# Performance work log

Measured on AMD Instinct MI355X. Metric: run time of the kernel, lower is better.

The kernel has to match this reference:

```python
import jax, jax.numpy as jnp
import numpy as np
from jax.ops import segment_sum

N, E, D, H = 50000, 800000, 128, 128


def setup_inputs() -> dict:
    key = jax.random.key(0)
    ks = jax.random.split(key, 8)
    x = jax.random.normal(ks[0], (N, D), dtype=jnp.float32)
    edge_index = jax.random.randint(ks[1], (2, E), 0, N, dtype=jnp.int64)
    # Glorot-ish scaled weights for 3 GCNConv layers
    s0 = 1.0 / np.sqrt(D)
    s1 = 1.0 / np.sqrt(H)
    W0 = jax.random.normal(ks[2], (D, H), dtype=jnp.float32) * s0
    W1 = jax.random.normal(ks[3], (H, H), dtype=jnp.float32) * s1
    W2 = jax.random.normal(ks[4], (H, H), dtype=jnp.float32) * s1
    b0 = jnp.zeros((H,), dtype=jnp.float32)
    b1 = jnp.zeros((H,), dtype=jnp.float32)
    b2 = jnp.zeros((H,), dtype=jnp.float32)
    return {"x": x, "edge_index": edge_index,
            "W0": W0, "b0": b0, "W1": W1, "b1": b1, "W2": W2, "b2": b2}


def _gcn_norm(edge_index, num_nodes):
    # Add self-loops, compute symmetric normalization deg^-1/2 A deg^-1/2
    loops = jnp.arange(num_nodes, dtype=edge_index.dtype)
    src = jnp.concatenate([edge_index[0], loops])  # [E+N]
    dst = jnp.concatenate([edge_index[1], loops])  # [E+N]
    deg = segment_sum(jnp.ones_like(dst, dtype=jnp.float32), dst,
                      num_segments=num_nodes)       # in-degree incl. self-loop
    dinv = jnp.where(deg > 0, jax.lax.rsqrt(deg), 0.0)
    norm = dinv[src] * dinv[dst]                    # [E+N]
    return src, dst, norm


def _gcn_conv(x, src, dst, norm, W, b, num_nodes):
    h = x @ W                                        # [N, H] linear first (PyG order)
    msg = h[src] * norm[:, None]                     # gather + scale
    agg = segment_sum(msg, dst, num_segments=num_nodes)  # scatter-add
    return agg + b


def reference(x, edge_index, W0, b0, W1, b1, W2, b2):
    num_nodes = x.shape[0]
    src, dst, norm = _gcn_norm(edge_index, num_nodes)
    for W, b in ((W0, b0), (W1, b1), (W2, b2)):
        x = jax.nn.relu(_gcn_conv(x, src, dst, norm, W, b, num_nodes))
    return x
```

## Files before the change

### kernel.cpp

```cpp
#include <hip/hip_runtime.h>


typedef __attribute__((ext_vector_type(8))) unsigned short ushort8;
typedef __attribute__((ext_vector_type(8))) short short8v;
typedef __attribute__((ext_vector_type(4))) float f32x4;

__device__ __forceinline__ unsigned short f2bf(float f) {
    unsigned u = __float_as_uint(f);
    unsigned r = (u + 0x7FFF + ((u >> 16) & 1)) >> 16;
    return (unsigned short)r;
}
__device__ __forceinline__ float bf2f(unsigned short s) {
    return __uint_as_float(((unsigned)s) << 16);
}

__global__ __launch_bounds__(256) void zero_kernel(int4* __restrict__ p, int n4) {
    int i = blockIdx.x * 256 + threadIdx.x;
    if (i < n4) p[i] = make_int4(0, 0, 0, 0);
}

__global__ void count_rank_kernel(const int* __restrict__ ei, int* __restrict__ cnt,
                                  int* __restrict__ rank, int E) {
    int e = (blockIdx.x * blockDim.x + threadIdx.x) * 4;
    if (e + 4 <= E) {
        int4 d4 = *(const int4*)(ei + E + e);
        int4 r;
        r.x = atomicAdd(&cnt[d4.x], 1);
        r.y = atomicAdd(&cnt[d4.y], 1);
        r.z = atomicAdd(&cnt[d4.z], 1);
        r.w = atomicAdd(&cnt[d4.w], 1);
        *(int4*)(rank + e) = r;
    } else {
        for (; e < E; ++e) rank[e] = atomicAdd(&cnt[ei[E + e]], 1);
    }
}

__global__ __launch_bounds__(256) void block_sum_kernel(const int* __restrict__ cnt,
                                                        int* __restrict__ bsum, int n) {
    int i = blockIdx.x * 256 + threadIdx.x;
    int v = (i < n) ? cnt[i] : 0;
#pragma unroll
    for (int off = 32; off; off >>= 1) v += __shfl_down(v, off);
    __shared__ int ws[4];
    int lane = threadIdx.x & 63, w = threadIdx.x >> 6;
    if (lane == 0) ws[w] = v;
    __syncthreads();
    if (threadIdx.x == 0) bsum[blockIdx.x] = ws[0] + ws[1] + ws[2] + ws[3];
}

__global__ __launch_bounds__(256) void scan_partials_kernel(const int* __restrict__ bsum,
                                                            int* __restrict__ bpre,
                                                            int* __restrict__ rowptr,
                                                            int nb, int n) {
    __shared__ int sh[256];
    int t = threadIdx.x;
    int v = (t < nb) ? bsum[t] : 0;
    sh[t] = v;
    __syncthreads();
    for (int off = 1; off < 256; off <<= 1) {
        int u = (t >= off) ? sh[t - off] : 0;
        __syncthreads();
        sh[t] += u;
        __syncthreads();
    }
    if (t < nb) bpre[t] = sh[t] - v;
    if (t == 255) rowptr[n] = sh[255];
}

__global__ __launch_bounds__(256) void scan_write_kernel(const int* __restrict__ cnt,
                                                         const int* __restrict__ bpre,
                                                         int* __restrict__ rowptr,
                                                         float* __restrict__ dinv, int n) {
    __shared__ int sh[256];
    int t = threadIdx.x;
    int i = blockIdx.x * 256 + t;
    int c = (i < n) ? cnt[i] : 0;
    sh[t] = c;
    __syncthreads();
    for (int off = 1; off < 256; off <<= 1) {
        int u = (t >= off) ? sh[t - off] : 0;
        __syncthreads();
        sh[t] += u;
        __syncthreads();
    }
    if (i < n) {
        rowptr[i] = bpre[blockIdx.x] + sh[t] - c;
        dinv[i] = rsqrtf((float)(c + 1));
    }
}

__global__ void fill_kernel(const int* __restrict__ ei, const int* __restrict__ rowptr,
                            const int* __restrict__ rank,
                            unsigned short* __restrict__ col, int E) {
    int e = (blockIdx.x * blockDim.x + threadIdx.x) * 4;
    if (e + 4 <= E) {
        int4 s4 = *(const int4*)(ei + e);
        int4 d4 = *(const int4*)(ei + E + e);
        int4 r4 = *(const int4*)(rank + e);
        col[rowptr[d4.x] + r4.x] = (unsigned short)s4.x;
        col[rowptr[d4.y] + r4.y] = (unsigned short)s4.y;
        col[rowptr[d4.z] + r4.z] = (unsigned short)s4.z;
        col[rowptr[d4.w] + r4.w] = (unsigned short)s4.w;
    } else {
        for (; e < E; ++e) col[rowptr[ei[E + e]] + rank[e]] = (unsigned short)ei[e];
    }
}

__global__ __launch_bounds__(256) void wprep_kernel(const float* __restrict__ W0,
                                                    const float* __restrict__ W1,
                                                    const float* __restrict__ W2,
                                                    short* __restrict__ F0,
                                                    short* __restrict__ F1,
                                                    short* __restrict__ F2) {
    int which = blockIdx.x >> 3;
    const float* W = which == 0 ? W0 : (which == 1 ? W1 : W2);
    short* Wfrag   = which == 0 ? F0 : (which == 1 ? F1 : F2);
    int idx = (blockIdx.x & 7) * 256 + threadIdx.x;
    int l = idx & 63;
    int cks = idx >> 6;
    int ks = cks & 3, c = cks >> 2;
    int col = c * 16 + (l & 15);
    int k0 = ks * 32 + (l >> 4) * 8;
    short8v o;
#pragma unroll
    for (int j = 0; j < 8; ++j) o[j] = (short)f2bf(W[(size_t)(k0 + j) * 128 + col]);
    ((short8v*)Wfrag)[idx] = o;
}

template <bool IN_BF16>
__global__ __launch_bounds__(256) void gemm_mfma_kernel(const void* __restrict__ Xv,
                                                        const short* __restrict__ Wfrag,
                                                        const float* __restrict__ dinv,
                                                        unsigned short* __restrict__ G, int n) {
    int t = threadIdx.x;
    int wv = t >> 6, l = t & 63;
    int row0 = blockIdx.x * 64 + wv * 16;
    int r = l & 15, half = l >> 4;
    int arow = row0 + r;
    bool rok = arow < n;

    f32x4 acc[8];
#pragma unroll
    for (int c = 0; c < 8; ++c) acc[c] = (f32x4){0.f, 0.f, 0.f, 0.f};

    const short8v* WF = (const short8v*)Wfrag;

#pragma unroll
    for (int ks = 0; ks < 4; ++ks) {
        short8v a = (short8v){0, 0, 0, 0, 0, 0, 0, 0};
        if (rok) {
            if (IN_BF16) {
                const unsigned short* X = (const unsigned short*)Xv;
                a = *(const short8v*)(X + (size_t)arow * 128 + ks * 32 + half * 8);
            } else {
                const float* X = (const float*)Xv;
                const float4* xp = (const float4*)(X + (size_t)arow * 128 + ks * 32 + half * 8);
                float4 x0 = xp[0], x1 = xp[1];
                a[0] = (short)f2bf(x0.x); a[1] = (short)f2bf(x0.y);
                a[2] = (short)f2bf(x0.z); a[3] = (short)f2bf(x0.w);
                a[4] = (short)f2bf(x1.x); a[5] = (short)f2bf(x1.y);
                a[6] = (short)f2bf(x1.z); a[7] = (short)f2bf(x1.w);
            }
        }
#pragma unroll
        for (int c = 0; c < 8; ++c) {
            short8v b = WF[(c * 4 + ks) * 64 + l];
            acc[c] = __builtin_amdgcn_mfma_f32_16x16x32_bf16(a, b, acc[c], 0, 0, 0);
        }
    }

    float ds[4];
    int orow[4];
#pragma unroll
    for (int i = 0; i < 4; ++i) {
        orow[i] = row0 + half * 4 + i;
        ds[i] = (orow[i] < n) ? dinv[orow[i]] : 0.f;
    }
#pragma unroll
    for (int c = 0; c < 8; ++c) {
#pragma unroll
        for (int i = 0; i < 4; ++i) {
            if (orow[i] < n)
                G[(size_t)orow[i] * 128 + c * 16 + r] = f2bf(ds[i] * acc[c][i]);
        }
    }
}

template <bool OUT_BF16>
__global__ __launch_bounds__(256) void agg_kernel(const unsigned short* __restrict__ G,
                                                  const int* __restrict__ rowptr,
                                                  const unsigned short* __restrict__ col,
                                                  const float* __restrict__ dinv,
                                                  const float* __restrict__ b,
                                                  void* __restrict__ outv, int n) {
    int gw = (int)((blockIdx.x * blockDim.x + threadIdx.x) >> 6);
    if (gw >= n) return;
    int lane = threadIdx.x & 63;
    int q = lane & 15, p = lane >> 4;
    int beg = rowptr[gw], end = rowptr[gw + 1];
    float di = dinv[gw];

    ushort8 gs = *(const ushort8*)(G + (size_t)gw * 128 + q * 8);

    float acc[8];
#pragma unroll
    for (int j = 0; j < 8; ++j) acc[j] = 0.f;

    int deg = end - beg;
    int nit = (deg + 7) >> 3;

    auto issue = [&](int s, ushort8& h0, ushort8& h1, float& m0, float& m1) {
        int i0 = beg + s * 8 + p;
        int i1 = i0 + 4;
        bool v0 = i0 < end, v1 = i1 < end;
        int c0 = col[v0 ? i0 : beg];
        int c1 = col[v1 ? i1 : beg];
        m0 = v0 ? 1.f : 0.f;
        m1 = v1 ? 1.f : 0.f;
        h0 = *(const ushort8*)(G + (size_t)c0 * 128 + q * 8);
        h1 = *(const ushort8*)(G + (size_t)c1 * 128 + q * 8);
    };

    ushort8 h0a = {}, h1a = {}, h0b = {}, h1b = {};
    float m0a = 0.f, m1a = 0.f, m0b = 0.f, m1b = 0.f;

    if (nit > 0) issue(0, h0a, h1a, m0a, m1a);
    if (nit > 1) issue(1, h0b, h1b, m0b, m1b);
    for (int s = 0; s < nit; ++s) {
#pragma unroll
        for (int j = 0; j < 8; ++j) {
            acc[j] = fmaf(m0a, bf2f(h0a[j]), acc[j]);
            acc[j] = fmaf(m1a, bf2f(h1a[j]), acc[j]);
        }
        h0a = h0b; h1a = h1b; m0a = m0b; m1a = m1b;
        if (s + 2 < nit) issue(s + 2, h0b, h1b, m0b, m1b);
    }

#pragma unroll
    for (int j = 0; j < 8; ++j) {
        acc[j] += __shfl_xor(acc[j], 16);
        acc[j] += __shfl_xor(acc[j], 32);
    }

    if (p == 0) {
        float4 b0 = *(const float4*)(b + q * 8);
        float4 b1 = *(const float4*)(b + q * 8 + 4);
        float o[8];
#pragma unroll
        for (int j = 0; j < 8; ++j) o[j] = di * (acc[j] + bf2f(gs[j]));
        o[0] += b0.x; o[1] += b0.y; o[2] += b0.z; o[3] += b0.w;
        o[4] += b1.x; o[5] += b1.y; o[6] += b1.z; o[7] += b1.w;
#pragma unroll
        for (int j = 0; j < 8; ++j) o[j] = fmaxf(o[j], 0.f);
        if (OUT_BF16) {
            ushort8 ov;
#pragma unroll
            for (int j = 0; j < 8; ++j) ov[j] = f2bf(o[j]);
            *(ushort8*)((unsigned short*)outv + (size_t)gw * 128 + q * 8) = ov;
        } else {
            float* out = (float*)outv;
            *(float4*)(out + (size_t)gw * 128 + q * 8)     = make_float4(o[0], o[1], o[2], o[3]);
            *(float4*)(out + (size_t)gw * 128 + q * 8 + 4) = make_float4(o[4], o[5], o[6], o[7]);
        }
    }
}

extern "C" void kernel_launch(void* const* d_in, const int* in_sizes, int n_in,
                              void* d_out, int out_size, void* d_ws, size_t ws_size,
                              hipStream_t stream) {
    const float* x  = (const float*)d_in[0];
    const int*   ei = (const int*)d_in[1];
    const float* W0 = (const float*)d_in[2];
    const float* b0 = (const float*)d_in[3];
    const float* W1 = (const float*)d_in[4];
    const float* b1 = (const float*)d_in[5];
    const float* W2 = (const float*)d_in[6];
    const float* b2 = (const float*)d_in[7];
    float* out = (float*)d_out;

    int N = in_sizes[0] / 128;
    int E = in_sizes[1] / 2;
    int nb = (N + 255) / 256;

    char* wsb = (char*)d_ws;
    size_t off = 0;
    auto alloc = [&](size_t bytes) -> void* {
        void* p = wsb + off;
        off = (off + bytes + 255) & ~(size_t)255;
        return p;
    };
    int*   cnt    = (int*)  alloc((size_t)N * 4);
    int*   rowptr = (int*)  alloc((size_t)(N + 1) * 4);
    float* dinv   = (float*)alloc((size_t)N * 4);
    int*   bsum   = (int*)  alloc((size_t)nb * 4);
    int*   bpre   = (int*)  alloc((size_t)nb * 4);
    int*   rank   = (int*)  alloc((size_t)E * 4);
    unsigned short* col = (unsigned short*)alloc((size_t)E * 2);
    unsigned short* g   = (unsigned short*)alloc((size_t)N * 128 * 2);
    unsigned short* xB  = (unsigned short*)alloc((size_t)N * 128 * 2);
    short* wf0    = (short*)alloc(128 * 128 * 2);
    short* wf1    = (short*)alloc(128 * 128 * 2);
    short* wf2    = (short*)alloc(128 * 128 * 2);

    int n4 = (N + 3) / 4;
    zero_kernel<<<(n4 + 255) / 256, 256, 0, stream>>>((int4*)cnt, n4);
    int e4 = (E + 3) / 4;
    count_rank_kernel<<<(e4 + 255) / 256, 256, 0, stream>>>(ei, cnt, rank, E);
    block_sum_kernel<<<nb, 256, 0, stream>>>(cnt, bsum, N);
    scan_partials_kernel<<<1, 256, 0, stream>>>(bsum, bpre, rowptr, nb, N);
    scan_write_kernel<<<nb, 256, 0, stream>>>(cnt, bpre, rowptr, dinv, N);
    fill_kernel<<<(e4 + 255) / 256, 256, 0, stream>>>(ei, rowptr, rank, col, E);
    wprep_kernel<<<24, 256, 0, stream>>>(W0, W1, W2, wf0, wf1, wf2);

    int gblk = (N + 63) / 64;
    int ablk = (N + 3) / 4;

    gemm_mfma_kernel<false><<<gblk, 256, 0, stream>>>(x,  wf0, dinv, g, N);
    agg_kernel<true><<<ablk, 256, 0, stream>>>(g, rowptr, col, dinv, b0, xB, N);

    gemm_mfma_kernel<true><<<gblk, 256, 0, stream>>>(xB, wf1, dinv, g, N);
    agg_kernel<true><<<ablk, 256, 0, stream>>>(g, rowptr, col, dinv, b1, xB, N);

    gemm_mfma_kernel<true><<<gblk, 256, 0, stream>>>(xB, wf2, dinv, g, N);
    agg_kernel<false><<<ablk, 256, 0, stream>>>(g, rowptr, col, dinv, b2, out, N);
}
```

Baseline: 214.9 us.

## Co-launch independent preprocessing stages to cut kernel launches and overlap work

```diff
diff --git a/kernel.cpp b/kernel.cpp
--- a/kernel.cpp
+++ b/kernel.cpp
@@ -14,14 +14,106 @@
     return __uint_as_float(((unsigned)s) << 16);
 }
 
-__global__ __launch_bounds__(256) void zero_kernel(int4* __restrict__ p, int n4) {
-    int i = blockIdx.x * 256 + threadIdx.x;
-    if (i < n4) p[i] = make_int4(0, 0, 0, 0);
-}
-
-__global__ void count_rank_kernel(const int* __restrict__ ei, int* __restrict__ cnt,
-                                  int* __restrict__ rank, int E) {
-    int e = (blockIdx.x * blockDim.x + threadIdx.x) * 4;
+__global__ __launch_bounds__(256) void prep0_kernel(int4* __restrict__ cntv, int n4, int zblk,
+                                                    const float* __restrict__ W0,
+                                                    const float* __restrict__ W1,
+                                                    const float* __restrict__ W2,
+                                                    short* __restrict__ F0,
+                                                    short* __restrict__ F1,
+                                                    short* __restrict__ F2) {
+    int bid = blockIdx.x;
+    if (bid < zblk) {
+        int i = bid * 256 + threadIdx.x;
+        if (i < n4) cntv[i] = make_int4(0, 0, 0, 0);
+        return;
+    }
+    int wb = bid - zblk;
+    int which = wb >> 3;
+    const float* W = which == 0 ? W0 : (which == 1 ? W1 : W2);
+    short* Wfrag   = which == 0 ? F0 : (which == 1 ? F1 : F2);
+    int idx = (wb & 7) * 256 + threadIdx.x;
+    int l = idx & 63;
+    int cks = idx >> 6;
+    int ks = cks & 3, c = cks >> 2;
+    int col = c * 16 + (l & 15);
+    int k0 = ks * 32 + (l >> 4) * 8;
+    short8v o;
+#pragma unroll
+    for (int j = 0; j < 8; ++j) o[j] = (short)f2bf(W[(size_t)(k0 + j) * 128 + col]);
+    ((short8v*)Wfrag)[idx] = o;
+}
+
+template <bool IN_BF16, bool SCALE>
+__device__ __forceinline__ void gemm_body(int bid, const void* __restrict__ Xv,
+                                          const short* __restrict__ Wfrag,
+                                          const float* __restrict__ dinv,
+                                          unsigned short* __restrict__ G, int n) {
+    int t = threadIdx.x;
+    int wv = t >> 6, l = t & 63;
+    int row0 = bid * 64 + wv * 16;
+    int r = l & 15, half = l >> 4;
+    int arow = row0 + r;
+    bool rok = arow < n;
+
+    f32x4 acc[8];
+#pragma unroll
+    for (int c = 0; c < 8; ++c) acc[c] = (f32x4){0.f, 0.f, 0.f, 0.f};
+
+    const short8v* WF = (const short8v*)Wfrag;
+
+#pragma unroll
+    for (int ks = 0; ks < 4; ++ks) {
+        short8v a = (short8v){0, 0, 0, 0, 0, 0, 0, 0};
+        if (rok) {
+            if (IN_BF16) {
+                const unsigned short* X = (const unsigned short*)Xv;
+                a = *(const short8v*)(X + (size_t)arow * 128 + ks * 32 + half * 8);
+            } else {
+                const float* X = (const float*)Xv;
+                const float4* xp = (const float4*)(X + (size_t)arow * 128 + ks * 32 + half * 8);
+                float4 x0 = xp[0], x1 = xp[1];
+                a[0] = (short)f2bf(x0.x); a[1] = (short)f2bf(x0.y);
+                a[2] = (short)f2bf(x0.z); a[3] = (short)f2bf(x0.w);
+                a[4] = (short)f2bf(x1.x); a[5] = (short)f2bf(x1.y);
+                a[6] = (short)f2bf(x1.z); a[7] = (short)f2bf(x1.w);
+            }
+        }
+#pragma unroll
+        for (int c = 0; c < 8; ++c) {
+            short8v b = WF[(c * 4 + ks) * 64 + l];
+            acc[c] = __builtin_amdgcn_mfma_f32_16x16x32_bf16(a, b, acc[c], 0, 0, 0);
+        }
+    }
+
+    float ds[4];
+    int orow[4];
+#pragma unroll
+    for (int i = 0; i < 4; ++i) {
+        orow[i] = row0 + half * 4 + i;
+        ds[i] = SCALE ? ((orow[i] < n) ? dinv[orow[i]] : 0.f) : 1.f;
+    }
+#pragma unroll
+    for (int c = 0; c < 8; ++c) {
+#pragma unroll
+        for (int i = 0; i < 4; ++i) {
+            if (orow[i] < n)
+                G[(size_t)orow[i] * 128 + c * 16 + r] = f2bf(ds[i] * acc[c][i]);
+        }
+    }
+}
+
+__global__ __launch_bounds__(256) void cg_kernel(const float* __restrict__ X,
+                                                 const short* __restrict__ Wfrag,
+                                                 unsigned short* __restrict__ H, int n, int gblk,
+                                                 const int* __restrict__ ei,
+                                                 int* __restrict__ cnt,
+                                                 int* __restrict__ rank, int E) {
+    int bid = blockIdx.x;
+    if (bid < gblk) {
+        gemm_body<false, false>(bid, X, Wfrag, nullptr, H, n);
+        return;
+    }
+    int e = ((bid - gblk) * 256 + threadIdx.x) * 4;
     if (e + 4 <= E) {
         int4 d4 = *(const int4*)(ei + E + e);
         int4 r;
@@ -33,6 +125,13 @@
     } else {
         for (; e < E; ++e) rank[e] = atomicAdd(&cnt[ei[E + e]], 1);
     }
+}
+
+__global__ __launch_bounds__(256) void gemm_mfma_kernel(const void* __restrict__ Xv,
+                                                        const short* __restrict__ Wfrag,
+                                                        const float* __restrict__ dinv,
+                                                        unsigned short* __restrict__ G, int n) {
+    gemm_body<true, true>(blockIdx.x, Xv, Wfrag, dinv, G, n);
 }
 
 __global__ __launch_bounds__(256) void block_sum_kernel(const int* __restrict__ cnt,
@@ -89,100 +188,39 @@
     }
 }
 
-__global__ void fill_kernel(const int* __restrict__ ei, const int* __restrict__ rowptr,
-                            const int* __restrict__ rank,
-                            unsigned short* __restrict__ col, int E) {
-    int e = (blockIdx.x * blockDim.x + threadIdx.x) * 4;
-    if (e + 4 <= E) {
-        int4 s4 = *(const int4*)(ei + e);
-        int4 d4 = *(const int4*)(ei + E + e);
-        int4 r4 = *(const int4*)(rank + e);
-        col[rowptr[d4.x] + r4.x] = (unsigned short)s4.x;
-        col[rowptr[d4.y] + r4.y] = (unsigned short)s4.y;
-        col[rowptr[d4.z] + r4.z] = (unsigned short)s4.z;
-        col[rowptr[d4.w] + r4.w] = (unsigned short)s4.w;
-    } else {
-        for (; e < E; ++e) col[rowptr[ei[E + e]] + rank[e]] = (unsigned short)ei[e];
-    }
-}
-
-__global__ __launch_bounds__(256) void wprep_kernel(const float* __restrict__ W0,
-                                                    const float* __restrict__ W1,
-                                                    const float* __restrict__ W2,
-                                                    short* __restrict__ F0,
-                                                    short* __restrict__ F1,
-                                                    short* __restrict__ F2) {
-    int which = blockIdx.x >> 3;
-    const float* W = which == 0 ? W0 : (which == 1 ? W1 : W2);
-    short* Wfrag   = which == 0 ? F0 : (which == 1 ? F1 : F2);
-    int idx = (blockIdx.x & 7) * 256 + threadIdx.x;
-    int l = idx & 63;
-    int cks = idx >> 6;
-    int ks = cks & 3, c = cks >> 2;
-    int col = c * 16 + (l & 15);
-    int k0 = ks * 32 + (l >> 4) * 8;
-    short8v o;
-#pragma unroll
-    for (int j = 0; j < 8; ++j) o[j] = (short)f2bf(W[(size_t)(k0 + j) * 128 + col]);
-    ((short8v*)Wfrag)[idx] = o;
-}
-
-template <bool IN_BF16>
-__global__ __launch_bounds__(256) void gemm_mfma_kernel(const void* __restrict__ Xv,
-                                                        const short* __restrict__ Wfrag,
+__global__ __launch_bounds__(256) void fillscale_kernel(const int* __restrict__ ei,
+                                                        const int* __restrict__ rowptr,
+                                                        const int* __restrict__ rank,
+                                                        unsigned short* __restrict__ col, int E,
+                                                        int fblk,
+                                                        const unsigned short* __restrict__ H,
                                                         const float* __restrict__ dinv,
                                                         unsigned short* __restrict__ G, int n) {
-    int t = threadIdx.x;
-    int wv = t >> 6, l = t & 63;
-    int row0 = blockIdx.x * 64 + wv * 16;
-    int r = l & 15, half = l >> 4;
-    int arow = row0 + r;
-    bool rok = arow < n;
-
-    f32x4 acc[8];
-#pragma unroll
-    for (int c = 0; c < 8; ++c) acc[c] = (f32x4){0.f, 0.f, 0.f, 0.f};
-
-    const short8v* WF = (const short8v*)Wfrag;
-
-#pragma unroll
-    for (int ks = 0; ks < 4; ++ks) {
-        short8v a = (short8v){0, 0, 0, 0, 0, 0, 0, 0};
-        if (rok) {
-            if (IN_BF16) {
-                const unsigned short* X = (const unsigned short*)Xv;
-                a = *(const short8v*)(X + (size_t)arow * 128 + ks * 32 + half * 8);
-            } else {
-                const float* X = (const float*)Xv;
-                const float4* xp = (const float4*)(X + (size_t)arow * 128 + ks * 32 + half * 8);
-                float4 x0 = xp[0], x1 = xp[1];
-                a[0] = (short)f2bf(x0.x); a[1] = (short)f2bf(x0.y);
-                a[2] = (short)f2bf(x0.z); a[3] = (short)f2bf(x0.w);
-                a[4] = (short)f2bf(x1.x); a[5] = (short)f2bf(x1.y);
-                a[6] = (short)f2bf(x1.z); a[7] = (short)f2bf(x1.w);
-            }
-        }
-#pragma unroll
-        for (int c = 0; c < 8; ++c) {
-            short8v b = WF[(c * 4 + ks) * 64 + l];
-            acc[c] = __builtin_amdgcn_mfma_f32_16x16x32_bf16(a, b, acc[c], 0, 0, 0);
-        }
-    }
-
-    float ds[4];
-    int orow[4];
-#pragma unroll
-    for (int i = 0; i < 4; ++i) {
-        orow[i] = row0 + half * 4 + i;
-        ds[i] = (orow[i] < n) ? dinv[orow[i]] : 0.f;
-    }
-#pragma unroll
-    for (int c = 0; c < 8; ++c) {
-#pragma unroll
-        for (int i = 0; i < 4; ++i) {
-            if (orow[i] < n)
-                G[(size_t)orow[i] * 128 + c * 16 + r] = f2bf(ds[i] * acc[c][i]);
-        }
+    int bid = blockIdx.x;
+    if (bid < fblk) {
+        int e = (bid * 256 + threadIdx.x) * 4;
+        if (e + 4 <= E) {
+            int4 s4 = *(const int4*)(ei + e);
+            int4 d4 = *(const int4*)(ei + E + e);
+            int4 r4 = *(const int4*)(rank + e);
+            col[rowptr[d4.x] + r4.x] = (unsigned short)s4.x;
+            col[rowptr[d4.y] + r4.y] = (unsigned short)s4.y;
+            col[rowptr[d4.z] + r4.z] = (unsigned short)s4.z;
+            col[rowptr[d4.w] + r4.w] = (unsigned short)s4.w;
+        } else {
+            for (; e < E; ++e) col[rowptr[ei[E + e]] + rank[e]] = (unsigned short)ei[e];
+        }
+        return;
+    }
+    int idx = (bid - fblk) * 256 + threadIdx.x;
+    int row = idx >> 4, q = idx & 15;
+    if (row < n) {
+        float d = dinv[row];
+        ushort8 h = *(const ushort8*)(H + (size_t)row * 128 + q * 8);
+        ushort8 o;
+#pragma unroll
+        for (int j = 0; j < 8; ++j) o[j] = f2bf(d * bf2f(h[j]));
+        *(ushort8*)(G + (size_t)row * 128 + q * 8) = o;
     }
 }
 
@@ -297,30 +335,35 @@
     int*   rank   = (int*)  alloc((size_t)E * 4);
     unsigned short* col = (unsigned short*)alloc((size_t)E * 2);
     unsigned short* g   = (unsigned short*)alloc((size_t)N * 128 * 2);
+    unsigned short* h   = (unsigned short*)alloc((size_t)N * 128 * 2);
     unsigned short* xB  = (unsigned short*)alloc((size_t)N * 128 * 2);
     short* wf0    = (short*)alloc(128 * 128 * 2);
     short* wf1    = (short*)alloc(128 * 128 * 2);
     short* wf2    = (short*)alloc(128 * 128 * 2);
 
     int n4 = (N + 3) / 4;
-    zero_kernel<<<(n4 + 255) / 256, 256, 0, stream>>>((int4*)cnt, n4);
+    int zblk = (n4 + 255) / 256;
+    int gblk = (N + 63) / 64;
     int e4 = (E + 3) / 4;
-    count_rank_kernel<<<(e4 + 255) / 256, 256, 0, stream>>>(ei, cnt, rank, E);
+    int cblk = (e4 + 255) / 256;
+    int fblk = cblk;
+    int sblk = (N * 16 + 255) / 256;
+    int ablk = (N + 3) / 4;
+
+    prep0_kernel<<<zblk + 24, 256, 0, stream>>>((int4*)cnt, n4, zblk,
+                                                W0, W1, W2, wf0, wf1, wf2);
+    cg_kernel<<<gblk + cblk, 256, 0, stream>>>(x, wf0, h, N, gblk, ei, cnt, rank, E);
     block_sum_kernel<<<nb, 256, 0, stream>>>(cnt, bsum, N);
     scan_partials_kernel<<<1, 256, 0, stream>>>(bsum, bpre, rowptr, nb, N);
     scan_write_kernel<<<nb, 256, 0, stream>>>(cnt, bpre, rowptr, dinv, N);
-    fill_kernel<<<(e4 + 255) / 256, 256, 0, stream>>>(ei, rowptr, rank, col, E);
-    wprep_kernel<<<24, 256, 0, stream>>>(W0, W1, W2, wf0, wf1, wf2);
-
-    int gblk = (N + 63) / 64;
-    int ablk = (N + 3) / 4;
-
-    gemm_mfma_kernel<false><<<gblk, 256, 0, stream>>>(x,  wf0, dinv, g, N);
+    fillscale_kernel<<<fblk + sblk, 256, 0, stream>>>(ei, rowptr, rank, col, E,
+                                                      fblk, h, dinv, g, N);
+
     agg_kernel<true><<<ablk, 256, 0, stream>>>(g, rowptr, col, dinv, b0, xB, N);
 
-    gemm_mfma_kernel<true><<<gblk, 256, 0, stream>>>(xB, wf1, dinv, g, N);
+    gemm_mfma_kernel<<<gblk, 256, 0, stream>>>(xB, wf1, dinv, g, N);
     agg_kernel<true><<<ablk, 256, 0, stream>>>(g, rowptr, col, dinv, b1, xB, N);
 
-    gemm_mfma_kernel<true><<<gblk, 256, 0, stream>>>(xB, wf2, dinv, g, N);
+    gemm_mfma_kernel<<<gblk, 256, 0, stream>>>(xB, wf2, dinv, g, N);
     agg_kernel<false><<<ablk, 256, 0, stream>>>(g, rowptr, col, dinv, b2, out, N);
 }
```

After: 205.7 us. 1.05x faster.
